# Kernel tuning notes

Hardware: AMD Instinct MI355X
Metric: run time of the kernel (lower is better)

## Reference

```python
import jax, jax.numpy as jnp
import numpy as np

D_MODEL = 128
NHEAD = 8
NLAYERS = 6
LAYER_NAMES = ['self', 'cross', 'self', 'cross', 'self', 'cross']
TEMPERATURE = 5.0
EPS = 1e-6


def _pos_encoding(x):
    # Sinusoidal 1D position encoding along the width axis. x: [N, H, W, C]
    C, W = x.shape[-1], x.shape[2]
    pos = jnp.arange(W, dtype=x.dtype)[:, None]                      # [W,1]
    div = jnp.exp(jnp.arange(0, C, 2, dtype=x.dtype) * (-np.log(10000.0) / C))
    pe = jnp.zeros((W, C), x.dtype)
    pe = pe.at[:, 0::2].set(jnp.sin(pos * div))
    pe = pe.at[:, 1::2].set(jnp.cos(pos * div))
    return x + pe[None, None]                                        # broadcast over N,H


def _linear_attention(q, k, v):
    # q,k,v: [N, H, W, nhead, dim]; kernelized linear attention along W
    Q = jax.nn.elu(q) + 1.0
    K = jax.nn.elu(k) + 1.0
    v_len = v.shape[2]
    V = v / v_len
    KV = jnp.einsum('nhsed,nhsev->nhedv', K, V)                      # [N,H,e,d,d]
    Z = 1.0 / (jnp.einsum('nhled,nhed->nhle', Q, K.sum(axis=2)) + EPS)
    return jnp.einsum('nhled,nhedv,nhle->nhlev', Q, KV, Z) * v_len


def _layer_norm(x, g, b):
    m = x.mean(-1, keepdims=True)
    v = jnp.mean((x - m) ** 2, -1, keepdims=True)
    return (x - m) / jnp.sqrt(v + 1e-5) * g + b


def _encoder_layer(x, source, Wq, Wk, Wv, Wm, W1, W2, g1, b1, g2, b2):
    x = _pos_encoding(x)
    source = _pos_encoding(source)
    bs, h, w, c = x.shape
    e, d = NHEAD, c // NHEAD
    q = (x @ Wq).reshape(bs, h, w, e, d)
    k = (source @ Wk).reshape(bs, h, w, e, d)
    v = (source @ Wv).reshape(bs, h, w, e, d)
    msg = _linear_attention(q, k, v).reshape(bs, h, w, c) @ Wm
    msg = _layer_norm(msg, g1, b1)
    msg = jnp.concatenate([x, msg], axis=-1)                         # [N,H,W,2C]
    msg = jax.nn.relu(msg @ W1) @ W2
    msg = _layer_norm(msg, g2, b2)
    return x + msg


def _forward(feat0, feat1, Wq, Wk, Wv, Wm, W1, W2, g1, b1, g2, b2):
    feat0 = feat0.transpose(0, 2, 3, 1)                              # [N,H,W,C]
    feat1 = feat1.transpose(0, 2, 3, 1)
    for i, name in enumerate(LAYER_NAMES):
        p = (Wq[i], Wk[i], Wv[i], Wm[i], W1[i], W2[i], g1[i], b1[i], g2[i], b2[i])
        if name == 'self':
            feat0 = _encoder_layer(feat0, feat0, *p)
            feat1 = _encoder_layer(feat1, feat1, *p)
        else:  # cross: sequential update (feat1 sees updated feat0), as in torch source
            feat0 = _encoder_layer(feat0, feat1, *p)
            feat1 = _encoder_layer(feat1, feat0, *p)
    w = feat0.shape[2]
    attn_mask = jnp.where(jnp.triu(jnp.ones((w, w), bool), 1), -jnp.inf, 0.0)
    attn_mask = attn_mask[None, None].astype(feat0.dtype)
    scale = feat0.shape[-1] ** 0.5
    sim = jnp.einsum('ntwc,ntlc->ntwl', feat0 / scale, feat1 / scale) / TEMPERATURE
    return sim + attn_mask


def setup_inputs() -> dict:
    key = jax.random.key(0)
    ks = jax.random.split(key, 12)
    N, C, H, W = 2, D_MODEL, 64, 640
    L, D = NLAYERS, D_MODEL
    s = 1.0 / np.sqrt(D)
    s2 = 1.0 / np.sqrt(2 * D)
    return {
        'feat0': jax.random.normal(ks[0], (N, C, H, W), jnp.float32),
        'feat1': jax.random.normal(ks[1], (N, C, H, W), jnp.float32),
        'Wq': jax.random.normal(ks[2], (L, D, D), jnp.float32) * s,
        'Wk': jax.random.normal(ks[3], (L, D, D), jnp.float32) * s,
        'Wv': jax.random.normal(ks[4], (L, D, D), jnp.float32) * s,
        'Wm': jax.random.normal(ks[5], (L, D, D), jnp.float32) * s,
        'W1': jax.random.normal(ks[6], (L, 2 * D, 2 * D), jnp.float32) * s2,
        'W2': jax.random.normal(ks[7], (L, 2 * D, D), jnp.float32) * s2,
        'g1': jnp.ones((L, D), jnp.float32),
        'b1': jnp.zeros((L, D), jnp.float32),
        'g2': jnp.ones((L, D), jnp.float32),
        'b2': jnp.zeros((L, D), jnp.float32),
    }


def reference(feat0, feat1, Wq, Wk, Wv, Wm, W1, W2, g1, b1, g2, b2):
    return _forward(feat0, feat1, Wq, Wk, Wv, Wm, W1, W2, g1, b1, g2, b2)
```

## Files before the change

### kernel.cpp

```cpp
#include <hip/hip_runtime.h>
#include <cmath>
#include <math.h>

#define TOK 81920
#define WDIM 640

typedef __attribute__((ext_vector_type(8))) short short8v;
typedef __attribute__((ext_vector_type(4))) float f32x4;

__device__ __forceinline__ short f2bf(float f) {
  union { float f; unsigned u; } x; x.f = f;
  unsigned r = (x.u + 0x7fffu + ((x.u >> 16) & 1u)) >> 16;
  return (short)r;
}
__device__ __forceinline__ float bf2f(short s) {
  union { unsigned u; float f; } x; x.u = ((unsigned)(unsigned short)s) << 16;
  return x.f;
}

__global__ __launch_bounds__(256) void pe_kernel(float* __restrict__ pe) {
  int id = blockIdx.x * 256 + threadIdx.x;
  if (id >= WDIM * 128) return;
  int w = id >> 7;
  int c = id & 127;
  float i2 = (float)(c & 126);
  float freq = expf(i2 * -0.071955784156063941f);
  float ang = (float)w * freq;
  pe[id] = (c & 1) ? cosf(ang) : sinf(ang);
}

__global__ __launch_bounds__(256) void tr_kernel(const float* __restrict__ in0,
                                                 const float* __restrict__ in1,
                                                 short* __restrict__ x0,
                                                 short* __restrict__ x1) {
  __shared__ float t[32][33];
  int w0 = blockIdx.x * 32;
  int c0 = blockIdx.y * 32;
  int z = blockIdx.z;
  int feat = z >> 7;
  int nh = z & 127;
  int n = nh >> 6, h = nh & 63;
  const float* in = feat ? in1 : in0;
  short* out = feat ? x1 : x0;
  int tx = threadIdx.x & 31, ty = threadIdx.x >> 5;
  const float* ip = in + ((n * 128 + c0) * 64 + h) * 640 + w0;
#pragma unroll
  for (int i = 0; i < 32; i += 8)
    t[ty + i][tx] = ip[(ty + i) * (64 * 640) + tx];
  __syncthreads();
  short* op = out + ((size_t)(n * 64 + h) * 640 + w0) * 128 + c0;
#pragma unroll
  for (int i = 0; i < 32; i += 8)
    op[(size_t)(ty + i) * 128 + tx] = f2bf(t[tx][ty + i]);
}

__global__ __launch_bounds__(256) void wprep_kernel(
    const float* __restrict__ Wq, const float* __restrict__ Wk,
    const float* __restrict__ Wv, const float* __restrict__ Wm,
    const float* __restrict__ W1, const float* __restrict__ W2,
    short* __restrict__ BT) {
  int id = blockIdx.x * 256 + threadIdx.x;
  if (id >= 6 * 163840) return;
  int layer = id / 163840;
  int r = id % 163840;
  float v;
  if (r < 65536) {
    int seg = r >> 14;
    int rr = r & 16383;
    int n = rr >> 7, k = rr & 127;
    const float* W = seg == 0 ? Wq : seg == 1 ? Wk : seg == 2 ? Wv : Wm;
    v = W[layer * 16384 + k * 128 + n];
  } else if (r < 131072) {
    int rr = r - 65536;
    int n = rr >> 8, k = rr & 255;
    v = W1[layer * 65536 + k * 256 + n];
  } else {
    int rr = r - 131072;
    int n = rr >> 8, k = rr & 255;
    v = W2[layer * 32768 + k * 128 + n];
  }
  BT[id] = f2bf(v);
}

__device__ __forceinline__ void load_af(const short* __restrict__ A,
                                        const float* __restrict__ pe,
                                        int bm, int wr, int l15, int lk,
                                        short8v af[4][4]) {
  const int wbase = bm % WDIM;
#pragma unroll
  for (int mf = 0; mf < 4; ++mf) {
    const int rl = wr * 64 + mf * 16 + l15;
    const short* ar = A + (size_t)(bm + rl) * 128;
    const float* pr = pe + (size_t)(wbase + rl) * 128;
#pragma unroll
    for (int ks = 0; ks < 4; ++ks) {
      const int kloc = ks * 32 + lk * 8;
      short8v xa = *(const short8v*)(ar + kloc);
      f32x4 p0 = *(const f32x4*)(pr + kloc);
      f32x4 p1 = *(const f32x4*)(pr + kloc + 4);
      short8v o;
      o[0] = f2bf(bf2f(xa[0]) + p0[0]); o[1] = f2bf(bf2f(xa[1]) + p0[1]);
      o[2] = f2bf(bf2f(xa[2]) + p0[2]); o[3] = f2bf(bf2f(xa[3]) + p0[3]);
      o[4] = f2bf(bf2f(xa[4]) + p1[0]); o[5] = f2bf(bf2f(xa[5]) + p1[1]);
      o[6] = f2bf(bf2f(xa[6]) + p1[2]); o[7] = f2bf(bf2f(xa[7]) + p1[3]);
      af[ks][mf] = o;
    }
  }
}

__device__ __forceinline__ void proj_pass(const short8v af[4][4],
                                          const short* __restrict__ WT,
                                          int bm, int wr, int wc, int l15, int lk,
                                          short* __restrict__ out) {
  f32x4 acc[4][4] = {};
#pragma unroll
  for (int ks = 0; ks < 4; ++ks) {
    const int kloc = ks * 32 + lk * 8;
    short8v bfr[4];
#pragma unroll
    for (int nf = 0; nf < 4; ++nf)
      bfr[nf] = *(const short8v*)&WT[(size_t)(wc * 64 + nf * 16 + l15) * 128 + kloc];
#pragma unroll
    for (int mf = 0; mf < 4; ++mf)
#pragma unroll
      for (int nf = 0; nf < 4; ++nf)
        acc[mf][nf] = __builtin_amdgcn_mfma_f32_16x16x32_bf16(
            af[ks][mf], bfr[nf], acc[mf][nf], 0, 0, 0);
  }
#pragma unroll
  for (int mf = 0; mf < 4; ++mf)
#pragma unroll
    for (int nf = 0; nf < 4; ++nf) {
      const int colL = wc * 64 + nf * 16 + l15;
#pragma unroll
      for (int r = 0; r < 4; ++r) {
        const int row = bm + wr * 64 + mf * 16 + lk * 4 + r;
        out[(size_t)row * 128 + colL] = f2bf(acc[mf][nf][r]);
      }
    }
}

__global__ __launch_bounds__(256) void qkv_self_kernel(
    const short* __restrict__ x0, const short* __restrict__ x1,
    const float* __restrict__ pe,
    const short* __restrict__ wqT, const short* __restrict__ wkT,
    const short* __restrict__ wvT,
    short* q0, short* k0, short* v0, short* q1, short* k1, short* v1) {
  const int tid = threadIdx.x, lane = tid & 63, wid = tid >> 6;
  const int wr = wid >> 1, wc = wid & 1;
  const int bm = blockIdx.x * 128;
  const int l15 = lane & 15, lk = lane >> 4;
  const int z = blockIdx.z;
  const short* A = z ? x1 : x0;
  short8v af[4][4];
  load_af(A, pe, bm, wr, l15, lk, af);
  proj_pass(af, wqT, bm, wr, wc, l15, lk, z ? q1 : q0);
  proj_pass(af, wkT, bm, wr, wc, l15, lk, z ? k1 : k0);
  proj_pass(af, wvT, bm, wr, wc, l15, lk, z ? v1 : v0);
}

__global__ __launch_bounds__(256) void qkv_cross_kernel(
    const short* __restrict__ xq, const short* __restrict__ xs,
    const float* __restrict__ pe,
    const short* __restrict__ wqT, const short* __restrict__ wkT,
    const short* __restrict__ wvT,
    short* qb, short* kb, short* vb) {
  const int tid = threadIdx.x, lane = tid & 63, wid = tid >> 6;
  const int wr = wid >> 1, wc = wid & 1;
  const int bm = blockIdx.x * 128;
  const int l15 = lane & 15, lk = lane >> 4;
  short8v af[4][4];
  if (blockIdx.y == 0) {
    load_af(xq, pe, bm, wr, l15, lk, af);
    proj_pass(af, wqT, bm, wr, wc, l15, lk, qb);
  } else {
    load_af(xs, pe, bm, wr, l15, lk, af);
    proj_pass(af, wkT, bm, wr, wc, l15, lk, kb);
    proj_pass(af, wvT, bm, wr, wc, l15, lk, vb);
  }
}

template <int DUAL>
__global__ __launch_bounds__(256) void attn_kernel(
    const short* q0, const short* __restrict__ k0, const short* __restrict__ v0,
    const short* q1, const short* __restrict__ k1, const short* __restrict__ v1) {
  const int fid = blockIdx.x;
  const int per8 = DUAL ? 32 : 16;
  const int c8 = fid & 7, kk_ = fid >> 3;
  const int s = c8 * per8 + (kk_ >> 3);
  const int e = kk_ & 7;
  const bool f1 = DUAL && (s >= 128);
  const short* qb = f1 ? q1 : q0;
  const short* kb = f1 ? k1 : k0;
  const short* vb = f1 ? v1 : v0;
  short* ob = const_cast<short*>(qb);
  const int nh = s & 127;
  const size_t base = (size_t)nh * (640 * 128) + e * 16;

  __shared__ float Ks[128][16];
  __shared__ float Vs[128][16];
  __shared__ float KVs[16][17];
  __shared__ float Ksum[16];
  const int tid = threadIdx.x;
  const int d = tid >> 4;
  const int vv = tid & 15;
  const int srow = tid >> 1, shalf = (tid & 1) * 8;
  float kv = 0.f, ks = 0.f;
  for (int s0 = 0; s0 < 640; s0 += 128) {
    short8v k8 = *(const short8v*)&kb[base + (size_t)(s0 + srow) * 128 + shalf];
    short8v v8 = *(const short8v*)&vb[base + (size_t)(s0 + srow) * 128 + shalf];
#pragma unroll
    for (int j = 0; j < 8; ++j) {
      float kr = bf2f(k8[j]);
      Ks[srow][shalf + j] = kr > 0.f ? kr + 1.f : __expf(kr);
      Vs[srow][shalf + j] = bf2f(v8[j]);
    }
    __syncthreads();
#pragma unroll 8
    for (int sl = 0; sl < 128; ++sl) {
      float kk = Ks[sl][d];
      kv = fmaf(kk, Vs[sl][vv], kv);
      ks += kk;
    }
    __syncthreads();
  }
  KVs[d][vv] = kv;
  if (vv == 0) Ksum[d] = ks;
  __syncthreads();
  const int lane = tid & 63;
  const int wv = tid >> 6;
  const int rr = lane >> 4;
  const int cc = lane & 15;
  float kvc[16], ksr[16];
#pragma unroll
  for (int dd = 0; dd < 16; ++dd) { kvc[dd] = KVs[dd][cc]; ksr[dd] = Ksum[dd]; }
  for (int l0 = wv * 4; l0 < 640; l0 += 16) {
    int l = l0 + rr;
    float qraw = bf2f(qb[base + (size_t)l * 128 + cc]);
    float qe = qraw > 0.f ? qraw + 1.f : __expf(qraw);
    float o = 0.f, dz = 0.f;
#pragma unroll
    for (int dd = 0; dd < 16; ++dd) {
      float qv = __shfl(qe, rr * 16 + dd);
      o = fmaf(qv, kvc[dd], o);
      dz = fmaf(qv, ksr[dd], dz);
    }
    ob[base + (size_t)l * 128 + cc] = f2bf(o / (dz + 1e-6f));
  }
}

__global__ __launch_bounds__(256) void wm_ln_kernel(
    short* oA, short* oB, const short* __restrict__ wmT,
    const float* __restrict__ g, const float* __restrict__ b) {
  const int z = blockIdx.z;
  short* o = z ? oB : oA;
  __shared__ float lds_s[2][128];
  __shared__ float lds_q[2][128];
  const int tid = threadIdx.x, lane = tid & 63, wid = tid >> 6;
  const int wr = wid >> 1, wc = wid & 1;
  const int bm = blockIdx.x * 128;
  const int l15 = lane & 15, lk = lane >> 4;
  f32x4 acc[4][4] = {};
#pragma unroll
  for (int ks = 0; ks < 4; ++ks) {
    const int kloc = ks * 32 + lk * 8;
    short8v bfr[4], afr[4];
#pragma unroll
    for (int nf = 0; nf < 4; ++nf)
      bfr[nf] = *(const short8v*)&wmT[(size_t)(wc * 64 + nf * 16 + l15) * 128 + kloc];
#pragma unroll
    for (int mf = 0; mf < 4; ++mf)
      afr[mf] = *(const short8v*)&o[(size_t)(bm + wr * 64 + mf * 16 + l15) * 128 + kloc];
#pragma unroll
    for (int mf = 0; mf < 4; ++mf)
#pragma unroll
      for (int nf = 0; nf < 4; ++nf)
        acc[mf][nf] = __builtin_amdgcn_mfma_f32_16x16x32_bf16(
            afr[mf], bfr[nf], acc[mf][nf], 0, 0, 0);
  }
#pragma unroll
  for (int mf = 0; mf < 4; ++mf)
#pragma unroll
    for (int r = 0; r < 4; ++r) {
      float s = acc[mf][0][r] + acc[mf][1][r] + acc[mf][2][r] + acc[mf][3][r];
      float qq = acc[mf][0][r] * acc[mf][0][r] + acc[mf][1][r] * acc[mf][1][r]
               + acc[mf][2][r] * acc[mf][2][r] + acc[mf][3][r] * acc[mf][3][r];
#pragma unroll
      for (int off = 1; off < 16; off <<= 1) {
        s += __shfl_xor(s, off);
        qq += __shfl_xor(qq, off);
      }
      if (l15 == 0) {
        int rl = wr * 64 + mf * 16 + lk * 4 + r;
        lds_s[wc][rl] = s;
        lds_q[wc][rl] = qq;
      }
    }
  __syncthreads();
  float gv[4], bv[4];
#pragma unroll
  for (int nf = 0; nf < 4; ++nf) {
    int c = wc * 64 + nf * 16 + l15;
    gv[nf] = g[c]; bv[nf] = b[c];
  }
#pragma unroll
  for (int mf = 0; mf < 4; ++mf)
#pragma unroll
    for (int r = 0; r < 4; ++r) {
      int rl = wr * 64 + mf * 16 + lk * 4 + r;
      float mean = (lds_s[0][rl] + lds_s[1][rl]) * (1.f / 128.f);
      float var = (lds_q[0][rl] + lds_q[1][rl]) * (1.f / 128.f) - mean * mean;
      float rstd = rsqrtf(var + 1e-5f);
#pragma unroll
      for (int nf = 0; nf < 4; ++nf) {
        float val = (acc[mf][nf][r] - mean) * rstd * gv[nf] + bv[nf];
        o[(size_t)(bm + rl) * 128 + wc * 64 + nf * 16 + l15] = f2bf(val);
      }
    }
}

__global__ __launch_bounds__(256) void w1_kernel(
    const short* __restrict__ xA, const short* __restrict__ xB,
    const short* __restrict__ mA, const short* __restrict__ mB,
    const float* __restrict__ pe, const short* __restrict__ w1T,
    short* h0A, short* h1A, short* h0B, short* h1B) {
  const int z = blockIdx.z;
  const short* x = z ? xB : xA;
  const short* m = z ? mB : mA;
  short* h0 = z ? h0B : h0A;
  short* h1 = z ? h1B : h1A;
  const int tid = threadIdx.x, lane = tid & 63, wid = tid >> 6;
  const int wr = wid >> 1, wc = wid & 1;
  const int bm = blockIdx.x * 128;
  const int l15 = lane & 15, lk = lane >> 4;
  const int wbase = bm % WDIM;
  for (int p = 0; p < 2; ++p) {
    f32x4 acc[4][4] = {};
#pragma unroll
    for (int ks = 0; ks < 8; ++ks) {
      const int kloc = ks * 32 + lk * 8;
      short8v bfr[4], afr[4];
#pragma unroll
      for (int nf = 0; nf < 4; ++nf)
        bfr[nf] = *(const short8v*)&w1T[(size_t)(p * 128 + wc * 64 + nf * 16 + l15) * 256 + kloc];
      if (ks < 4) {
#pragma unroll
        for (int mf = 0; mf < 4; ++mf) {
          const int rl = wr * 64 + mf * 16 + l15;
          short8v xa = *(const short8v*)(x + (size_t)(bm + rl) * 128 + kloc);
          const float* pr = pe + (size_t)(wbase + rl) * 128 + kloc;
          f32x4 p0 = *(const f32x4*)pr;
          f32x4 p1 = *(const f32x4*)(pr + 4);
          short8v ov;
          ov[0] = f2bf(bf2f(xa[0]) + p0[0]); ov[1] = f2bf(bf2f(xa[1]) + p0[1]);
          ov[2] = f2bf(bf2f(xa[2]) + p0[2]); ov[3] = f2bf(bf2f(xa[3]) + p0[3]);
          ov[4] = f2bf(bf2f(xa[4]) + p1[0]); ov[5] = f2bf(bf2f(xa[5]) + p1[1]);
          ov[6] = f2bf(bf2f(xa[6]) + p1[2]); ov[7] = f2bf(bf2f(xa[7]) + p1[3]);
          afr[mf] = ov;
        }
      } else {
#pragma unroll
        for (int mf = 0; mf < 4; ++mf)
          afr[mf] = *(const short8v*)&m[(size_t)(bm + wr * 64 + mf * 16 + l15) * 128 + kloc - 128];
      }
#pragma unroll
      for (int mf = 0; mf < 4; ++mf)
#pragma unroll
        for (int nf = 0; nf < 4; ++nf)
          acc[mf][nf] = __builtin_amdgcn_mfma_f32_16x16x32_bf16(
              afr[mf], bfr[nf], acc[mf][nf], 0, 0, 0);
    }
    short* h = p ? h1 : h0;
#pragma unroll
    for (int mf = 0; mf < 4; ++mf)
#pragma unroll
      for (int nf = 0; nf < 4; ++nf) {
        const int colL = wc * 64 + nf * 16 + l15;
#pragma unroll
        for (int r = 0; r < 4; ++r) {
          const int row = bm + wr * 64 + mf * 16 + lk * 4 + r;
          h[(size_t)row * 128 + colL] = f2bf(fmaxf(acc[mf][nf][r], 0.f));
        }
      }
  }
}

__global__ __launch_bounds__(256) void w2_ln_kernel(
    const short* __restrict__ h0A, const short* __restrict__ h1A,
    const short* __restrict__ h0B, const short* __restrict__ h1B,
    const short* __restrict__ w2T, short* xA, short* xB,
    const float* __restrict__ pe, const float* __restrict__ g,
    const float* __restrict__ b) {
  const int z = blockIdx.z;
  const short* h0 = z ? h0B : h0A;
  const short* h1 = z ? h1B : h1A;
  short* x = z ? xB : xA;
  __shared__ float lds_s[2][128];
  __shared__ float lds_q[2][128];
  const int tid = threadIdx.x, lane = tid & 63, wid = tid >> 6;
  const int wr = wid >> 1, wc = wid & 1;
  const int bm = blockIdx.x * 128;
  const int l15 = lane & 15, lk = lane >> 4;
  const int wbase = bm % WDIM;
  f32x4 acc[4][4] = {};
#pragma unroll
  for (int ks = 0; ks < 8; ++ks) {
    const int kloc = ks * 32 + lk * 8;
    const short* hp = (ks < 4) ? h0 : h1;
    const int kl = (ks < 4) ? kloc : kloc - 128;
    short8v bfr[4], afr[4];
#pragma unroll
    for (int nf = 0; nf < 4; ++nf)
      bfr[nf] = *(const short8v*)&w2T[(size_t)(wc * 64 + nf * 16 + l15) * 256 + kloc];
#pragma unroll
    for (int mf = 0; mf < 4; ++mf)
      afr[mf] = *(const short8v*)&hp[(size_t)(bm + wr * 64 + mf * 16 + l15) * 128 + kl];
#pragma unroll
    for (int mf = 0; mf < 4; ++mf)
#pragma unroll
      for (int nf = 0; nf < 4; ++nf)
        acc[mf][nf] = __builtin_amdgcn_mfma_f32_16x16x32_bf16(
            afr[mf], bfr[nf], acc[mf][nf], 0, 0, 0);
  }
#pragma unroll
  for (int mf = 0; mf < 4; ++mf)
#pragma unroll
    for (int r = 0; r < 4; ++r) {
      float s = acc[mf][0][r] + acc[mf][1][r] + acc[mf][2][r] + acc[mf][3][r];
      float qq = acc[mf][0][r] * acc[mf][0][r] + acc[mf][1][r] * acc[mf][1][r]
               + acc[mf][2][r] * acc[mf][2][r] + acc[mf][3][r] * acc[mf][3][r];
#pragma unroll
      for (int off = 1; off < 16; off <<= 1) {
        s += __shfl_xor(s, off);
        qq += __shfl_xor(qq, off);
      }
      if (l15 == 0) {
        int rl = wr * 64 + mf * 16 + lk * 4 + r;
        lds_s[wc][rl] = s;
        lds_q[wc][rl] = qq;
      }
    }
  __syncthreads();
  float gv[4], bv[4];
#pragma unroll
  for (int nf = 0; nf < 4; ++nf) {
    int c = wc * 64 + nf * 16 + l15;
    gv[nf] = g[c]; bv[nf] = b[c];
  }
#pragma unroll
  for (int mf = 0; mf < 4; ++mf)
#pragma unroll
    for (int r = 0; r < 4; ++r) {
      int rl = wr * 64 + mf * 16 + lk * 4 + r;
      float mean = (lds_s[0][rl] + lds_s[1][rl]) * (1.f / 128.f);
      float var = (lds_q[0][rl] + lds_q[1][rl]) * (1.f / 128.f) - mean * mean;
      float rstd = rsqrtf(var + 1e-5f);
      int row = bm + rl;
#pragma unroll
      for (int nf = 0; nf < 4; ++nf) {
        int col = wc * 64 + nf * 16 + l15;
        float ln = (acc[mf][nf][r] - mean) * rstd * gv[nf] + bv[nf];
        size_t xi = (size_t)row * 128 + col;
        float xv = bf2f(x[xi]) + pe[(size_t)(wbase + rl) * 128 + col] + ln;
        x[xi] = f2bf(xv);
      }
    }
}

__global__ __launch_bounds__(256) void sim_mfma(const short* __restrict__ f0,
                                                const short* __restrict__ f1,
                                                float* __restrict__ out) {
  const int fid = (blockIdx.z * 5 + blockIdx.y) * 5 + blockIdx.x;
  const int c8 = fid & 7, kk_ = fid >> 3;
  const int nt = c8 * 16 + kk_ / 25;
  const int r2 = kk_ % 25;
  const int bw = (r2 % 5) * 128;
  const int bl = (r2 / 5) * 128;
  const int tid = threadIdx.x;
  const int lane = tid & 63;
  const int wid = tid >> 6;
  const int wr = wid >> 1, wc = wid & 1;
  const short* __restrict__ A = f0 + (size_t)nt * 640 * 128;
  const short* __restrict__ B = f1 + (size_t)nt * 640 * 128;
  const int l15 = lane & 15;
  const int lk = lane >> 4;
  f32x4 acc[4][4] = {};
#pragma unroll
  for (int ks = 0; ks < 4; ++ks) {
    const int kloc = ks * 32 + lk * 8;
    short8v afr[4], bfr[4];
#pragma unroll
    for (int mf = 0; mf < 4; ++mf)
      afr[mf] = *(const short8v*)&A[(size_t)(bw + wr * 64 + mf * 16 + l15) * 128 + kloc];
#pragma unroll
    for (int nf = 0; nf < 4; ++nf)
      bfr[nf] = *(const short8v*)&B[(size_t)(bl + wc * 64 + nf * 16 + l15) * 128 + kloc];
#pragma unroll
    for (int mf = 0; mf < 4; ++mf)
#pragma unroll
      for (int nf = 0; nf < 4; ++nf)
        acc[mf][nf] = __builtin_amdgcn_mfma_f32_16x16x32_bf16(
            afr[mf], bfr[nf], acc[mf][nf], 0, 0, 0);
  }
#pragma unroll
  for (int mf = 0; mf < 4; ++mf)
#pragma unroll
    for (int nf = 0; nf < 4; ++nf) {
      const int l = bl + wc * 64 + nf * 16 + l15;
#pragma unroll
      for (int r = 0; r < 4; ++r) {
        const int w = bw + wr * 64 + mf * 16 + lk * 4 + r;
        float v = acc[mf][nf][r] * (1.f / 640.f);
        if (l > w) v = -1e30f;
        out[((size_t)nt * 640 + w) * 640 + l] = v;
      }
    }
}

extern "C" void kernel_launch(void* const* d_in, const int* in_sizes, int n_in,
                              void* d_out, int out_size, void* d_ws, size_t ws_size,
                              hipStream_t stream) {
  (void)in_sizes; (void)n_in; (void)out_size; (void)ws_size;
  const float* feat0 = (const float*)d_in[0];
  const float* feat1 = (const float*)d_in[1];
  const float* Wq = (const float*)d_in[2];
  const float* Wk = (const float*)d_in[3];
  const float* Wv = (const float*)d_in[4];
  const float* Wm = (const float*)d_in[5];
  const float* W1 = (const float*)d_in[6];
  const float* W2 = (const float*)d_in[7];
  const float* g1 = (const float*)d_in[8];
  const float* b1 = (const float*)d_in[9];
  const float* g2 = (const float*)d_in[10];
  const float* b2 = (const float*)d_in[11];

  float* wsf = (float*)d_ws;
  const size_t U = (size_t)TOK * 128;
  float* pe = wsf;
  short* x0 = (short*)(wsf + 81920);
  short* x1 = x0 + U;
  short* q0 = x1 + U;
  short* k0 = q0 + U;
  short* v0 = k0 + U;
  short* q1 = v0 + U;
  short* k1 = q1 + U;
  short* v1 = k1 + U;
  short* bt = v1 + U;

  dim3 blk(256);
  pe_kernel<<<dim3(320), blk, 0, stream>>>(pe);
  tr_kernel<<<dim3(20, 4, 256), blk, 0, stream>>>(feat0, feat1, x0, x1);
  wprep_kernel<<<dim3((6 * 163840 + 255) / 256), blk, 0, stream>>>(
      Wq, Wk, Wv, Wm, W1, W2, bt);

  const int NB = TOK / 128;
  for (int i = 0; i < 6; ++i) {
    const short* bt_i = bt + (size_t)i * 163840;
    const short* wqT = bt_i;
    const short* wkT = bt_i + 16384;
    const short* wvT = bt_i + 32768;
    const short* wmT = bt_i + 49152;
    const short* w1T = bt_i + 65536;
    const short* w2T = bt_i + 131072;
    const float* g1_i = g1 + i * 128;
    const float* b1_i = b1 + i * 128;
    const float* g2_i = g2 + i * 128;
    const float* b2_i = b2 + i * 128;
    if ((i & 1) == 0) {
      qkv_self_kernel<<<dim3(NB, 1, 2), blk, 0, stream>>>(
          x0, x1, pe, wqT, wkT, wvT, q0, k0, v0, q1, k1, v1);
      attn_kernel<1><<<dim3(2048), blk, 0, stream>>>(q0, k0, v0, q1, k1, v1);
      wm_ln_kernel<<<dim3(NB, 1, 2), blk, 0, stream>>>(q0, q1, wmT, g1_i, b1_i);
      w1_kernel<<<dim3(NB, 1, 2), blk, 0, stream>>>(
          x0, x1, q0, q1, pe, w1T, k0, v0, k1, v1);
      w2_ln_kernel<<<dim3(NB, 1, 2), blk, 0, stream>>>(
          k0, v0, k1, v1, w2T, x0, x1, pe, g2_i, b2_i);
    } else {
      qkv_cross_kernel<<<dim3(NB, 2), blk, 0, stream>>>(
          x0, x1, pe, wqT, wkT, wvT, q0, k0, v0);
      attn_kernel<0><<<dim3(1024), blk, 0, stream>>>(q0, k0, v0, q0, k0, v0);
      wm_ln_kernel<<<dim3(NB, 1, 1), blk, 0, stream>>>(q0, q0, wmT, g1_i, b1_i);
      w1_kernel<<<dim3(NB, 1, 1), blk, 0, stream>>>(
          x0, x0, q0, q0, pe, w1T, k0, v0, k0, v0);
      w2_ln_kernel<<<dim3(NB, 1, 1), blk, 0, stream>>>(
          k0, v0, k0, v0, w2T, x0, x0, pe, g2_i, b2_i);

      qkv_cross_kernel<<<dim3(NB, 2), blk, 0, stream>>>(
          x1, x0, pe, wqT, wkT, wvT, q0, k0, v0);
      attn_kernel<0><<<dim3(1024), blk, 0, stream>>>(q0, k0, v0, q0, k0, v0);
      wm_ln_kernel<<<dim3(NB, 1, 1), blk, 0, stream>>>(q0, q0, wmT, g1_i, b1_i);
      w1_kernel<<<dim3(NB, 1, 1), blk, 0, stream>>>(
          x1, x1, q0, q0, pe, w1T, k0, v0, k0, v0);
      w2_ln_kernel<<<dim3(NB, 1, 1), blk, 0, stream>>>(
          k0, v0, k0, v0, w2T, x1, x1, pe, g2_i, b2_i);
    }
  }
  sim_mfma<<<dim3(5, 5, 128), blk, 0, stream>>>(x0, x1, (float*)d_out);
}
```

Before: 2.806 ms.

## Split linear attention into chunked KV-reduction and vectorized apply kernels

```diff
diff --git a/kernel.cpp b/kernel.cpp
--- a/kernel.cpp
+++ b/kernel.cpp
@@ -180,73 +180,104 @@
   }
 }
 
-template <int DUAL>
-__global__ __launch_bounds__(256) void attn_kernel(
-    const short* q0, const short* __restrict__ k0, const short* __restrict__ v0,
-    const short* q1, const short* __restrict__ k1, const short* __restrict__ v1) {
-  const int fid = blockIdx.x;
-  const int per8 = DUAL ? 32 : 16;
-  const int c8 = fid & 7, kk_ = fid >> 3;
-  const int s = c8 * per8 + (kk_ >> 3);
-  const int e = kk_ & 7;
-  const bool f1 = DUAL && (s >= 128);
-  const short* qb = f1 ? q1 : q0;
-  const short* kb = f1 ? k1 : k0;
-  const short* vb = f1 ? v1 : v0;
-  short* ob = const_cast<short*>(qb);
-  const int nh = s & 127;
-  const size_t base = (size_t)nh * (640 * 128) + e * 16;
-
+template <int NSC>
+__global__ __launch_bounds__(256) void kv_kernel(
+    const short* __restrict__ k0, const short* __restrict__ v0,
+    const short* __restrict__ k1, const short* __restrict__ v1,
+    float* __restrict__ kvp) {
+  const int bid = blockIdx.x;
+  const int sc = bid % NSC;
+  const int e = bid / NSC;
+  const int strip = sc / 5, chunk = sc % 5;
+  const short* kb = (strip >= 128) ? k1 : k0;
+  const short* vb = (strip >= 128) ? v1 : v0;
+  const int nh = strip & 127;
+  const size_t base = (size_t)nh * (640 * 128) + (size_t)chunk * (128 * 128) + e * 16;
   __shared__ float Ks[128][16];
   __shared__ float Vs[128][16];
-  __shared__ float KVs[16][17];
-  __shared__ float Ksum[16];
   const int tid = threadIdx.x;
-  const int d = tid >> 4;
-  const int vv = tid & 15;
   const int srow = tid >> 1, shalf = (tid & 1) * 8;
+  short8v k8 = *(const short8v*)&kb[base + (size_t)srow * 128 + shalf];
+  short8v v8 = *(const short8v*)&vb[base + (size_t)srow * 128 + shalf];
+#pragma unroll
+  for (int j = 0; j < 8; ++j) {
+    float kr = bf2f(k8[j]);
+    Ks[srow][shalf + j] = kr > 0.f ? kr + 1.f : __expf(kr);
+    Vs[srow][shalf + j] = bf2f(v8[j]);
+  }
+  __syncthreads();
+  const int d = tid >> 4, vv = tid & 15;
   float kv = 0.f, ks = 0.f;
-  for (int s0 = 0; s0 < 640; s0 += 128) {
-    short8v k8 = *(const short8v*)&kb[base + (size_t)(s0 + srow) * 128 + shalf];
-    short8v v8 = *(const short8v*)&vb[base + (size_t)(s0 + srow) * 128 + shalf];
-#pragma unroll
-    for (int j = 0; j < 8; ++j) {
-      float kr = bf2f(k8[j]);
-      Ks[srow][shalf + j] = kr > 0.f ? kr + 1.f : __expf(kr);
-      Vs[srow][shalf + j] = bf2f(v8[j]);
-    }
-    __syncthreads();
 #pragma unroll 8
-    for (int sl = 0; sl < 128; ++sl) {
-      float kk = Ks[sl][d];
-      kv = fmaf(kk, Vs[sl][vv], kv);
-      ks += kk;
-    }
-    __syncthreads();
-  }
-  KVs[d][vv] = kv;
-  if (vv == 0) Ksum[d] = ks;
+  for (int sl = 0; sl < 128; ++sl) {
+    float kk = Ks[sl][d];
+    kv = fmaf(kk, Vs[sl][vv], kv);
+    ks += kk;
+  }
+  float* out = kvp + ((size_t)(strip * 8 + e) * 5 + chunk) * 272;
+  out[d * 16 + vv] = kv;
+  if (vv == 0) out[256 + d] = ks;
+}
+
+template <int DUAL>
+__global__ __launch_bounds__(256) void apply_kernel(
+    short* q0, short* q1, const float* __restrict__ kvp) {
+  const int bid = blockIdx.x;
+  const int strip = bid / 10, lc = bid % 10;
+  __shared__ float KV8[8][16][17];
+  __shared__ float KS8[8][16];
+  const int tid = threadIdx.x;
+  for (int idx = tid; idx < 8 * 272; idx += 256) {
+    int e = idx / 272, r = idx - e * 272;
+    const float* p = kvp + ((size_t)(strip * 8 + e) * 5) * 272 + r;
+    float s = ((p[0] + p[272]) + (p[544] + p[816])) + p[1088];
+    if (r < 256) KV8[e][r >> 4][r & 15] = s;
+    else         KS8[e][r - 256] = s;
+  }
   __syncthreads();
-  const int lane = tid & 63;
-  const int wv = tid >> 6;
-  const int rr = lane >> 4;
-  const int cc = lane & 15;
-  float kvc[16], ksr[16];
-#pragma unroll
-  for (int dd = 0; dd < 16; ++dd) { kvc[dd] = KVs[dd][cc]; ksr[dd] = Ksum[dd]; }
-  for (int l0 = wv * 4; l0 < 640; l0 += 16) {
-    int l = l0 + rr;
-    float qraw = bf2f(qb[base + (size_t)l * 128 + cc]);
-    float qe = qraw > 0.f ? qraw + 1.f : __expf(qraw);
-    float o = 0.f, dz = 0.f;
-#pragma unroll
-    for (int dd = 0; dd < 16; ++dd) {
-      float qv = __shfl(qe, rr * 16 + dd);
-      o = fmaf(qv, kvc[dd], o);
-      dz = fmaf(qv, ksr[dd], dz);
-    }
-    ob[base + (size_t)l * 128 + cc] = f2bf(o / (dz + 1e-6f));
-  }
+  short* qb = (DUAL && strip >= 128) ? q1 : q0;
+  const int nh = strip & 127;
+  const int row = lc * 64 + (tid >> 2);
+  const int cb = (tid & 3) * 32;
+  short* qp = qb + (size_t)nh * (640 * 128) + (size_t)row * 128 + cb;
+  short8v qv0 = *(const short8v*)(qp);
+  short8v qv1 = *(const short8v*)(qp + 8);
+  short8v qv2 = *(const short8v*)(qp + 16);
+  short8v qv3 = *(const short8v*)(qp + 24);
+  float qe[32];
+#pragma unroll
+  for (int j = 0; j < 8; ++j) {
+    float a = bf2f(qv0[j]); qe[j]      = a > 0.f ? a + 1.f : __expf(a);
+    float b = bf2f(qv1[j]); qe[8 + j]  = b > 0.f ? b + 1.f : __expf(b);
+    float c = bf2f(qv2[j]); qe[16 + j] = c > 0.f ? c + 1.f : __expf(c);
+    float d = bf2f(qv3[j]); qe[24 + j] = d > 0.f ? d + 1.f : __expf(d);
+  }
+  short res[32];
+#pragma unroll
+  for (int h = 0; h < 2; ++h) {
+    const int e = (cb >> 4) + h;
+    const float* Q = qe + h * 16;
+    float dz = 0.f;
+#pragma unroll
+    for (int dd = 0; dd < 16; ++dd) dz = fmaf(Q[dd], KS8[e][dd], dz);
+    const float zi = 1.f / (dz + 1e-6f);
+#pragma unroll
+    for (int vv = 0; vv < 16; ++vv) {
+      float o = 0.f;
+#pragma unroll
+      for (int dd = 0; dd < 16; ++dd) o = fmaf(Q[dd], KV8[e][dd][vv], o);
+      res[h * 16 + vv] = f2bf(o * zi);
+    }
+  }
+  short8v w0, w1, w2, w3;
+#pragma unroll
+  for (int j = 0; j < 8; ++j) {
+    w0[j] = res[j]; w1[j] = res[8 + j]; w2[j] = res[16 + j]; w3[j] = res[24 + j];
+  }
+  *(short8v*)(qp)      = w0;
+  *(short8v*)(qp + 8)  = w1;
+  *(short8v*)(qp + 16) = w2;
+  *(short8v*)(qp + 24) = w3;
 }
 
 __global__ __launch_bounds__(256) void wm_ln_kernel(
@@ -546,6 +577,7 @@
   short* k1 = q1 + U;
   short* v1 = k1 + U;
   short* bt = v1 + U;
+  float* kvp = (float*)(bt + 983040);
 
   dim3 blk(256);
   pe_kernel<<<dim3(320), blk, 0, stream>>>(pe);
@@ -569,7 +601,8 @@
     if ((i & 1) == 0) {
       qkv_self_kernel<<<dim3(NB, 1, 2), blk, 0, stream>>>(
           x0, x1, pe, wqT, wkT, wvT, q0, k0, v0, q1, k1, v1);
-      attn_kernel<1><<<dim3(2048), blk, 0, stream>>>(q0, k0, v0, q1, k1, v1);
+      kv_kernel<1280><<<dim3(8 * 1280), blk, 0, stream>>>(k0, v0, k1, v1, kvp);
+      apply_kernel<1><<<dim3(2560), blk, 0, stream>>>(q0, q1, kvp);
       wm_ln_kernel<<<dim3(NB, 1, 2), blk, 0, stream>>>(q0, q1, wmT, g1_i, b1_i);
       w1_kernel<<<dim3(NB, 1, 2), blk, 0, stream>>>(
           x0, x1, q0, q1, pe, w1T, k0, v0, k1, v1);
@@ -578,7 +611,8 @@
     } else {
       qkv_cross_kernel<<<dim3(NB, 2), blk, 0, stream>>>(
           x0, x1, pe, wqT, wkT, wvT, q0, k0, v0);
-      attn_kernel<0><<<dim3(1024), blk, 0, stream>>>(q0, k0, v0, q0, k0, v0);
+      kv_kernel<640><<<dim3(8 * 640), blk, 0, stream>>>(k0, v0, k0, v0, kvp);
+      apply_kernel<0><<<dim3(1280), blk, 0, stream>>>(q0, q0, kvp);
       wm_ln_kernel<<<dim3(NB, 1, 1), blk, 0, stream>>>(q0, q0, wmT, g1_i, b1_i);
       w1_kernel<<<dim3(NB, 1, 1), blk, 0, stream>>>(
           x0, x0, q0, q0, pe, w1T, k0, v0, k0, v0);
@@ -587,7 +621,8 @@
 
       qkv_cross_kernel<<<dim3(NB, 2), blk, 0, stream>>>(
           x1, x0, pe, wqT, wkT, wvT, q0, k0, v0);
-      attn_kernel<0><<<dim3(1024), blk, 0, stream>>>(q0, k0, v0, q0, k0, v0);
+      kv_kernel<640><<<dim3(8 * 640), blk, 0, stream>>>(k0, v0, k0, v0, kvp);
+      apply_kernel<0><<<dim3(1280), blk, 0, stream>>>(q0, q0, kvp);
       wm_ln_kernel<<<dim3(NB, 1, 1), blk, 0, stream>>>(q0, q0, wmT, g1_i, b1_i);
       w1_kernel<<<dim3(NB, 1, 1), blk, 0, stream>>>(
           x1, x1, q0, q0, pe, w1T, k0, v0, k0, v0);
```

Measured after the change: 2.846 ms. About the same (+1.4%).
